# Kernel optimization log

Measured on AMD Instinct MI355X. Metric: run time of the kernel, lower is better.

## Reference

```python
import math
import jax, jax.numpy as jnp
import numpy as np

EMB = 1024
HEADS = 16
HEAD_DIM = EMB // HEADS


def setup_inputs() -> dict:
    key = jax.random.key(0)
    ks = jax.random.split(key, 6)
    b, l = 4, 4096
    x = jax.random.normal(ks[0], (b, l, EMB), dtype=jnp.float32)
    # torch Linear weight shape (out, in); xavier_normal std = sqrt(2/(in+out))
    std = math.sqrt(2.0 / (EMB + EMB))
    Wq = jax.random.normal(ks[1], (EMB, EMB), dtype=jnp.float32) * std
    Wk = jax.random.normal(ks[2], (EMB, EMB), dtype=jnp.float32) * std
    Wv = jax.random.normal(ks[3], (EMB, EMB), dtype=jnp.float32) * std
    Wu = jax.random.normal(ks[4], (EMB, EMB), dtype=jnp.float32) * std
    Wo = jax.random.normal(ks[5], (EMB, EMB), dtype=jnp.float32) * std
    return {"x": x, "Wq": Wq, "Wk": Wk, "Wv": Wv, "Wu": Wu, "Wo": Wo}


def _srms_norm(x, eps=1e-12):
    # SRMSNorm over last dim with scale 1/sqrt(head_dims), computed in fp32
    dtype = x.dtype
    xf = x.astype(jnp.float32)
    scale = 1.0 / math.sqrt(x.shape[-1])
    n = jnp.linalg.norm(xf * scale, axis=-1, keepdims=True)
    return (xf / jnp.maximum(n, eps)).astype(dtype)


def reference(x, Wq, Wk, Wv, Wu, Wo):
    b, l, d = x.shape
    h, hd = HEADS, HEAD_DIM
    scale = math.sqrt(hd)

    def proj(W):
        return jnp.einsum('bld,ed->ble', x, W).reshape(b, l, h, hd).transpose(0, 2, 1, 3)

    q = jax.nn.relu(proj(Wq)) / scale        # (b,h,l,hd)
    k = jax.nn.relu(proj(Wk)) / scale
    v = proj(Wv)
    u = jax.nn.silu(proj(Wu))

    kv = jnp.einsum('bhlk,bhlv->bhkv', k, v)  # (b,h,hd,hd) state
    out = jnp.einsum('bhlk,bhkv->bhlv', q, kv)
    out = _srms_norm(out) * u
    out = out.transpose(0, 2, 1, 3).reshape(b, l, d)
    return jnp.einsum('bld,ed->ble', out, Wo)
```

## Files before the change

kernel.cpp:

```cpp
#include <hip/hip_runtime.h>

typedef _Float16 f16;
typedef _Float16 f16x4 __attribute__((ext_vector_type(4)));
typedef _Float16 f16x8 __attribute__((ext_vector_type(8)));
typedef float f32x4 __attribute__((ext_vector_type(4)));

#define EMB 1024
#define SEQL 4096
#define BATCH 4
#define NH 16
#define HD 64
#define BH 64
#define MROWS 16384
#define KVSPLIT 4

#define GLOAD_LDS(gp, lp) \
    __builtin_amdgcn_global_load_lds((const __attribute__((address_space(1))) void*)(gp), \
                                     (__attribute__((address_space(3))) void*)(lp), 16, 0, 0)

struct WPtrs { const float* p[5]; };

#define NXB (MROWS * EMB / 4 / 256)
#define NWB (5 * EMB * EMB / 4 / 256)
#define NZB (BH * HD * HD / 4 / 256)
__global__ void prep_kernel(const float* __restrict__ x, WPtrs wp,
                            f16* __restrict__ x16, f16* __restrict__ w16,
                            float4* __restrict__ kvz)
{
    int gid = blockIdx.x;
    int t = threadIdx.x;
    if (gid < NXB) {
        int i = gid * 256 + t;
        float4 v = ((const float4*)x)[i];
        f16x4 o = { (f16)v.x, (f16)v.y, (f16)v.z, (f16)v.w };
        ((f16x4*)x16)[i] = o;
    } else if (gid < NXB + NWB) {
        int i = (gid - NXB) * 256 + t;
        int wsel = i >> 18;
        int j = i & 262143;
        float4 v = ((const float4*)wp.p[wsel])[j];
        f16x4 o = { (f16)v.x, (f16)v.y, (f16)v.z, (f16)v.w };
        ((f16x4*)(w16 + (size_t)wsel * EMB * EMB))[j] = o;
    } else {
        int i = (gid - NXB - NWB) * 256 + t;
        kvz[i] = float4{0.f, 0.f, 0.f, 0.f};
    }
}


#define FENCE asm volatile("" ::: "memory")
#define WAITV(N) asm volatile("s_waitcnt vmcnt(" #N ")" ::: "memory")
#define BAR do { FENCE; __builtin_amdgcn_s_barrier(); FENCE; } while (0)

template<int MODE>
__global__ __launch_bounds__(512, 2) void gemm_kernel(
    const f16* __restrict__ A, const f16* __restrict__ Bt,
    void* __restrict__ Cv, int M, int N, int K)
{
    __shared__ f16 As[2][256 * 64];
    __shared__ f16 Bs[2][256 * 64];

    const int tid  = threadIdx.x;
    const int lane = tid & 63;
    const int w    = tid >> 6;
    const int rw   = lane & 15;
    const int quad = lane >> 4;
    const int wm   = w >> 2;
    const int wn   = w & 3;

    const f16* Ap = A;
    const f16* Bp = Bt;
    char* Cp = (char*)Cv;
    bool sel_qu = true;
    int m0, n0;
    if (MODE == 34) {
        int bid = blockIdx.x;
        if (bid < 512) {
            m0 = (bid >> 3) * 256; n0 = (bid & 7) * 256;
        } else {
            bid -= 512;
            m0 = (bid >> 6) * 256; n0 = (bid & 63) * 256;
            Ap = Bt + (size_t)2 * EMB * EMB;
            Bp = A;
            Cp = (char*)Cv + (size_t)2 * MROWS * EMB * 2;
            sel_qu = false;
        }
    } else {
        m0 = blockIdx.y * 256; n0 = blockIdx.x * 256;
    }
    const size_t Ks = (size_t)K;
    const int NT = K >> 6;

    const int srow8 = lane >> 3;
    const int slog  = (lane & 7) ^ srow8;
    const f16* gA = Ap + (size_t)(m0 + w * 8 + srow8) * Ks + slog * 8;
    const f16* gB = Bp + (size_t)(n0 + w * 8 + srow8) * Ks + slog * 8;
    const int lst = w * 512;

#define STAGE_A(H, T, BUF) do { \
    GLOAD_LDS(gA + (size_t)((H) * 128 +  0) * Ks + (T) * 64, &As[BUF][(H) * 8192 + lst]); \
    GLOAD_LDS(gA + (size_t)((H) * 128 + 64) * Ks + (T) * 64, &As[BUF][(H) * 8192 + 4096 + lst]); \
} while (0)
#define STAGE_B(H, T, BUF) do { \
    GLOAD_LDS(gB + (size_t)((H) * 128 +  0) * Ks + (T) * 64, &Bs[BUF][(H) * 8192 + lst]); \
    GLOAD_LDS(gB + (size_t)((H) * 128 + 64) * Ks + (T) * 64, &Bs[BUF][(H) * 8192 + 4096 + lst]); \
} while (0)

    const int rw7   = rw & 7;
    const int s0o   = ( quad      ^ rw7) * 8;
    const int s1o   = ((quad + 4) ^ rw7) * 8;
    const int abase = (wm * 64 + rw) * 64;
    const int bbase = (wn * 32 + rw) * 64;

    f32x4 acc[2][2][4][2] = {};
    f16x8 af[4][2], bf[2][2];

#define READ_A(QM, BUF) do { \
    _Pragma("unroll") \
    for (int mi = 0; mi < 4; ++mi) { \
        af[mi][0] = *(const f16x8*)&As[BUF][(QM) * 8192 + abase + mi * 1024 + s0o]; \
        af[mi][1] = *(const f16x8*)&As[BUF][(QM) * 8192 + abase + mi * 1024 + s1o]; \
    } \
} while (0)
#define READ_B(QN, BUF) do { \
    _Pragma("unroll") \
    for (int nj = 0; nj < 2; ++nj) { \
        bf[nj][0] = *(const f16x8*)&Bs[BUF][(QN) * 8192 + bbase + nj * 1024 + s0o]; \
        bf[nj][1] = *(const f16x8*)&Bs[BUF][(QN) * 8192 + bbase + nj * 1024 + s1o]; \
    } \
} while (0)
#define MFMA_Q(QM, QN) do { \
    __builtin_amdgcn_s_setprio(1); \
    _Pragma("unroll") \
    for (int mi = 0; mi < 4; ++mi) \
        _Pragma("unroll") \
        for (int nj = 0; nj < 2; ++nj) { \
            acc[QM][QN][mi][nj] = __builtin_amdgcn_mfma_f32_16x16x32_f16(bf[nj][0], af[mi][0], acc[QM][QN][mi][nj], 0, 0, 0); \
            acc[QM][QN][mi][nj] = __builtin_amdgcn_mfma_f32_16x16x32_f16(bf[nj][1], af[mi][1], acc[QM][QN][mi][nj], 0, 0, 0); \
        } \
    __builtin_amdgcn_s_setprio(0); \
} while (0)

    STAGE_A(0, 0, 0);
    STAGE_B(0, 0, 0);
    STAGE_B(1, 0, 0);
    STAGE_A(1, 0, 0);
    if (NT > 1) { STAGE_A(0, 1, 1); WAITV(2); } else { WAITV(0); }
    BAR;

    for (int kt = 0; kt < NT; ++kt) {
        const int cur = kt & 1, nxt = cur ^ 1;
        const bool p1 = (kt + 1 < NT), p2 = (kt + 2 < NT);
        READ_A(0, cur); READ_B(0, cur);
        if (p1) STAGE_B(0, kt + 1, nxt);
        BAR; MFMA_Q(0, 0); BAR;
        READ_B(1, cur);
        if (p1) { STAGE_B(1, kt + 1, nxt); WAITV(6); } else { WAITV(0); }
        BAR; MFMA_Q(0, 1); BAR;
        READ_A(1, cur);
        if (p1) STAGE_A(1, kt + 1, nxt);
        BAR; MFMA_Q(1, 1); BAR;
        READ_B(0, cur);
        if (p2) { STAGE_A(0, kt + 2, cur); WAITV(4); }
        else if (p1) { WAITV(2); }
        BAR; MFMA_Q(1, 0); BAR;
    }

    #pragma unroll
    for (int qm = 0; qm < 2; ++qm)
    #pragma unroll
    for (int qn = 0; qn < 2; ++qn)
    #pragma unroll
    for (int mi = 0; mi < 4; ++mi)
    #pragma unroll
    for (int nj = 0; nj < 2; ++nj) {
        const int m_idx = m0 + qm * 128 + wm * 64 + mi * 16 + rw;
        const int n_idx = n0 + qn * 128 + wn * 32 + nj * 16 + quad * 4;
        f32x4 a = acc[qm][qn][mi][nj];
        if (MODE == 0) {
            float4 vv = { a[0], a[1], a[2], a[3] };
            *(float4*)&((float*)Cv)[(size_t)m_idx * N + n_idx] = vv;
        } else if (sel_qu) {
            int sel = n_idx >> 10, e = n_idx & 1023;
            int b = m_idx >> 12, l = m_idx & 4095, h = e >> 6, hdi = e & 63;
            f16x4 o;
            #pragma unroll
            for (int r = 0; r < 4; r++) {
                float v = a[r];
                o[r] = (f16)(sel ? (v / (1.0f + __expf(-v))) : (fmaxf(v, 0.0f) * 0.125f));
            }
            *(f16x4*)&((f16*)Cp)[(size_t)sel * MROWS * EMB +
                                 (((size_t)(b * 16 + h) * 4096 + l) << 6) + hdi] = o;
        } else {
            int sel = m_idx >> 10, e = m_idx & 1023;
            int b = n_idx >> 12, l = n_idx & 4095;
            f16x4 o;
            #pragma unroll
            for (int r = 0; r < 4; r++) {
                float v = a[r];
                o[r] = (f16)(sel ? v : (fmaxf(v, 0.0f) * 0.125f));
            }
            *(f16x4*)&((f16*)Cp)[(size_t)sel * MROWS * EMB +
                                 (((size_t)b * 1024 + e) << 12) + l] = o;
        }
    }
#undef STAGE_A
#undef STAGE_B
#undef READ_A
#undef READ_B
#undef MFMA_Q
}

__global__ __launch_bounds__(256) void kv_split_kernel(
    const f16* __restrict__ kT, const f16* __restrict__ vT, float* __restrict__ kv32)
{
    const int bh    = blockIdx.x;
    const int chunk = blockIdx.y;
    const int lane  = threadIdx.x & 63;
    const int w     = threadIdx.x >> 6;
    const int rw    = lane & 15;
    const int quad  = lane >> 4;
    const int lbase = chunk * (SEQL / KVSPLIT);

    const f16* kp = kT + (size_t)bh * HD * SEQL + (size_t)(w * 16 + rw) * SEQL + lbase + quad * 8;
    const f16* vp = vT + (size_t)bh * HD * SEQL + (size_t)rw * SEQL + lbase + quad * 8;

    f32x4 acc[4] = {};
    for (int k0 = 0; k0 < SEQL / KVSPLIT; k0 += 32) {
        f16x8 a = *(const f16x8*)(kp + k0);
        #pragma unroll
        for (int t = 0; t < 4; t++) {
            f16x8 b = *(const f16x8*)(vp + (size_t)16 * t * SEQL + k0);
            acc[t] = __builtin_amdgcn_mfma_f32_16x16x32_f16(a, b, acc[t], 0, 0, 0);
        }
    }
    float* out = kv32 + (size_t)bh * HD * HD;
    #pragma unroll
    for (int t = 0; t < 4; t++)
        #pragma unroll
        for (int r = 0; r < 4; r++)
            atomicAdd(&out[(w * 16 + quad * 4 + r) * 64 + t * 16 + rw], acc[t][r]);
}

__global__ __launch_bounds__(256) void ret_out_kernel(
    const f16* __restrict__ q, const f16* __restrict__ u,
    const float* __restrict__ kv32, f16* __restrict__ o)
{
    const int bh    = blockIdx.x;
    const int chunk = blockIdx.y;
    const int lane  = threadIdx.x & 63;
    const int w     = threadIdx.x >> 6;
    const int rw    = lane & 15;
    const int quad  = lane >> 4;

    const float* kvp = kv32 + (size_t)bh * 4096;
    f16x8 bf[2][4];
    #pragma unroll
    for (int s = 0; s < 2; s++)
        #pragma unroll
        for (int t = 0; t < 4; t++)
            #pragma unroll
            for (int j = 0; j < 8; j++)
                bf[s][t][j] = (f16)kvp[(s * 32 + quad * 8 + j) * 64 + t * 16 + rw];

    const f16* qp = q + (size_t)bh * SEQL * HD;
    const f16* up = u + (size_t)bh * SEQL * HD;
    const int b = bh >> 4, h = bh & 15;
    f16* op = o + (size_t)b * SEQL * EMB + h * 64;

    const int l_wave = chunk * 512 + w * 128;
    for (int s = 0; s < 8; s++) {
        const int l0 = l_wave + s * 16;
        f16x8 a0 = *(const f16x8*)(qp + (size_t)(l0 + rw) * 64 + quad * 8);
        f16x8 a1 = *(const f16x8*)(qp + (size_t)(l0 + rw) * 64 + 32 + quad * 8);
        f32x4 acc[4] = {};
        #pragma unroll
        for (int t = 0; t < 4; t++) {
            acc[t] = __builtin_amdgcn_mfma_f32_16x16x32_f16(bf[0][t], a0, acc[t], 0, 0, 0);
            acc[t] = __builtin_amdgcn_mfma_f32_16x16x32_f16(bf[1][t], a1, acc[t], 0, 0, 0);
        }
        float ss = 0.f;
        #pragma unroll
        for (int t = 0; t < 4; t++)
            #pragma unroll
            for (int r = 0; r < 4; r++)
                ss += acc[t][r] * acc[t][r];
        ss += __shfl_xor(ss, 16);
        ss += __shfl_xor(ss, 32);
        const float inv = 8.0f / fmaxf(sqrtf(ss), 8e-12f);
        #pragma unroll
        for (int t = 0; t < 4; t++) {
            const int col = t * 16 + quad * 4;
            f16x4 uv = *(const f16x4*)(up + (size_t)(l0 + rw) * 64 + col);
            f16x4 o4;
            #pragma unroll
            for (int r = 0; r < 4; r++)
                o4[r] = (f16)(acc[t][r] * inv * (float)uv[r]);
            *(f16x4*)&op[(size_t)(l0 + rw) * EMB + col] = o4;
        }
    }
}

extern "C" void kernel_launch(void* const* d_in, const int* in_sizes, int n_in,
                              void* d_out, int out_size, void* d_ws, size_t ws_size,
                              hipStream_t stream)
{
    const float* x = (const float*)d_in[0];
    WPtrs wp;
    wp.p[0] = (const float*)d_in[1];
    wp.p[1] = (const float*)d_in[4];
    wp.p[2] = (const float*)d_in[2];
    wp.p[3] = (const float*)d_in[3];
    wp.p[4] = (const float*)d_in[5];

    char* ws = (char*)d_ws;
    size_t off = 0;
    f16* x16 = (f16*)(ws + off); off += (size_t)MROWS * EMB * 2;
    f16* w16 = (f16*)(ws + off); off += (size_t)5 * EMB * EMB * 2;
    f16* qb  = (f16*)(ws + off); off += (size_t)MROWS * EMB * 2;
    f16* ub  = (f16*)(ws + off); off += (size_t)MROWS * EMB * 2;
    f16* kTb = (f16*)(ws + off); off += (size_t)MROWS * EMB * 2;
    f16* vTb = (f16*)(ws + off); off += (size_t)MROWS * EMB * 2;
    float* kv32 = (float*)(ws + off); off += (size_t)BH * HD * HD * 4;
    f16* ob  = x16;
    (void)ub; (void)vTb;

    prep_kernel<<<NXB + NWB + NZB, 256, 0, stream>>>(x, wp, x16, w16, (float4*)kv32);

    f16* Wo = w16 + (size_t)4 * EMB * EMB;

    gemm_kernel<34><<<1024, 512, 0, stream>>>(x16, w16, qb, MROWS, 2 * EMB, EMB);

    kv_split_kernel<<<dim3(BH, KVSPLIT), dim3(256), 0, stream>>>(kTb, vTb, kv32);
    ret_out_kernel<<<dim3(BH, 8), dim3(256), 0, stream>>>(qb, ub, kv32, ob);

    gemm_kernel<0><<<dim3(4, 64), dim3(512), 0, stream>>>(ob, Wo, d_out, MROWS, EMB, EMB);
}
```

Before: 374.3 us.

## Fuse KV reduction, retention output and Wo GEMM into one cooperative kernel

Replaces the kv_split, ret_out and final output GEMM launches with a single cooperative tail kernel of 256 blocks x 512 threads. Grid-wide syncs separate the three phases: atomic KV-state accumulation, the normalized q·kv times u product, and the Wo projection with an LDS double-buffered MFMA loop. This is meant to remove inter-kernel launch gaps and tail effects. In exchange it adds two grid barriers, and it relies on every block being co-resident, given 128KB of static LDS per block.

```diff
diff --git a/kernel.cpp b/kernel.cpp
--- a/kernel.cpp
+++ b/kernel.cpp
@@ -1,4 +1,7 @@
 #include <hip/hip_runtime.h>
+#include <hip/hip_cooperative_groups.h>
+
+namespace cg = cooperative_groups;
 
 typedef _Float16 f16;
 typedef _Float16 f16x4 __attribute__((ext_vector_type(4)));
@@ -12,7 +15,6 @@
 #define HD 64
 #define BH 64
 #define MROWS 16384
-#define KVSPLIT 4
 
 #define GLOAD_LDS(gp, lp) \
     __builtin_amdgcn_global_load_lds((const __attribute__((address_space(1))) void*)(gp), \
@@ -211,93 +213,199 @@
 #undef MFMA_Q
 }
 
-__global__ __launch_bounds__(256) void kv_split_kernel(
-    const f16* __restrict__ kT, const f16* __restrict__ vT, float* __restrict__ kv32)
+__global__ __launch_bounds__(512, 2) void tail_kernel(
+    const f16* __restrict__ kT, const f16* __restrict__ vT, float* __restrict__ kv32,
+    const f16* __restrict__ q, const f16* __restrict__ u, f16* __restrict__ ob,
+    const f16* __restrict__ Wo, float* __restrict__ outp)
 {
-    const int bh    = blockIdx.x;
-    const int chunk = blockIdx.y;
-    const int lane  = threadIdx.x & 63;
-    const int w     = threadIdx.x >> 6;
-    const int rw    = lane & 15;
-    const int quad  = lane >> 4;
-    const int lbase = chunk * (SEQL / KVSPLIT);
-
-    const f16* kp = kT + (size_t)bh * HD * SEQL + (size_t)(w * 16 + rw) * SEQL + lbase + quad * 8;
-    const f16* vp = vT + (size_t)bh * HD * SEQL + (size_t)rw * SEQL + lbase + quad * 8;
-
-    f32x4 acc[4] = {};
-    for (int k0 = 0; k0 < SEQL / KVSPLIT; k0 += 32) {
-        f16x8 a = *(const f16x8*)(kp + k0);
-        #pragma unroll
-        for (int t = 0; t < 4; t++) {
-            f16x8 b = *(const f16x8*)(vp + (size_t)16 * t * SEQL + k0);
-            acc[t] = __builtin_amdgcn_mfma_f32_16x16x32_f16(a, b, acc[t], 0, 0, 0);
-        }
-    }
-    float* out = kv32 + (size_t)bh * HD * HD;
-    #pragma unroll
-    for (int t = 0; t < 4; t++)
-        #pragma unroll
-        for (int r = 0; r < 4; r++)
-            atomicAdd(&out[(w * 16 + quad * 4 + r) * 64 + t * 16 + rw], acc[t][r]);
-}
-
-__global__ __launch_bounds__(256) void ret_out_kernel(
-    const f16* __restrict__ q, const f16* __restrict__ u,
-    const float* __restrict__ kv32, f16* __restrict__ o)
-{
-    const int bh    = blockIdx.x;
-    const int chunk = blockIdx.y;
-    const int lane  = threadIdx.x & 63;
-    const int w     = threadIdx.x >> 6;
-    const int rw    = lane & 15;
-    const int quad  = lane >> 4;
-
-    const float* kvp = kv32 + (size_t)bh * 4096;
-    f16x8 bf[2][4];
-    #pragma unroll
-    for (int s = 0; s < 2; s++)
-        #pragma unroll
-        for (int t = 0; t < 4; t++)
-            #pragma unroll
-            for (int j = 0; j < 8; j++)
-                bf[s][t][j] = (f16)kvp[(s * 32 + quad * 8 + j) * 64 + t * 16 + rw];
-
-    const f16* qp = q + (size_t)bh * SEQL * HD;
-    const f16* up = u + (size_t)bh * SEQL * HD;
-    const int b = bh >> 4, h = bh & 15;
-    f16* op = o + (size_t)b * SEQL * EMB + h * 64;
-
-    const int l_wave = chunk * 512 + w * 128;
-    for (int s = 0; s < 8; s++) {
-        const int l0 = l_wave + s * 16;
-        f16x8 a0 = *(const f16x8*)(qp + (size_t)(l0 + rw) * 64 + quad * 8);
-        f16x8 a1 = *(const f16x8*)(qp + (size_t)(l0 + rw) * 64 + 32 + quad * 8);
-        f32x4 acc[4] = {};
-        #pragma unroll
-        for (int t = 0; t < 4; t++) {
-            acc[t] = __builtin_amdgcn_mfma_f32_16x16x32_f16(bf[0][t], a0, acc[t], 0, 0, 0);
-            acc[t] = __builtin_amdgcn_mfma_f32_16x16x32_f16(bf[1][t], a1, acc[t], 0, 0, 0);
-        }
-        float ss = 0.f;
-        #pragma unroll
-        for (int t = 0; t < 4; t++)
+    __shared__ f16 As[2][256 * 64];
+    __shared__ f16 Bs[2][256 * 64];
+
+    const int tid  = threadIdx.x;
+    const int lane = tid & 63;
+    const int w    = tid >> 6;
+    const int rw   = lane & 15;
+    const int quad = lane >> 4;
+    const int bid  = blockIdx.x;
+    const int bh   = bid >> 2;
+    const int c    = bid & 3;
+
+    {
+        const int mg = w >> 1, nh = w & 1;
+        const int lbase = c * 1024;
+        const f16* kp = kT + (size_t)bh * HD * SEQL + (size_t)(mg * 16 + rw) * SEQL + lbase + quad * 8;
+        const f16* vp = vT + (size_t)bh * HD * SEQL + (size_t)rw * SEQL + lbase + quad * 8;
+        f32x4 acc[2] = {};
+        for (int k0 = 0; k0 < 1024; k0 += 32) {
+            f16x8 a = *(const f16x8*)(kp + k0);
+            #pragma unroll
+            for (int t = 0; t < 2; t++) {
+                f16x8 b = *(const f16x8*)(vp + (size_t)16 * (nh * 2 + t) * SEQL + k0);
+                acc[t] = __builtin_amdgcn_mfma_f32_16x16x32_f16(a, b, acc[t], 0, 0, 0);
+            }
+        }
+        float* o = kv32 + (size_t)bh * HD * HD;
+        #pragma unroll
+        for (int t = 0; t < 2; t++)
             #pragma unroll
             for (int r = 0; r < 4; r++)
-                ss += acc[t][r] * acc[t][r];
-        ss += __shfl_xor(ss, 16);
-        ss += __shfl_xor(ss, 32);
-        const float inv = 8.0f / fmaxf(sqrtf(ss), 8e-12f);
-        #pragma unroll
-        for (int t = 0; t < 4; t++) {
-            const int col = t * 16 + quad * 4;
-            f16x4 uv = *(const f16x4*)(up + (size_t)(l0 + rw) * 64 + col);
-            f16x4 o4;
-            #pragma unroll
-            for (int r = 0; r < 4; r++)
-                o4[r] = (f16)(acc[t][r] * inv * (float)uv[r]);
-            *(f16x4*)&op[(size_t)(l0 + rw) * EMB + col] = o4;
-        }
+                atomicAdd(&o[(mg * 16 + quad * 4 + r) * 64 + (nh * 2 + t) * 16 + rw], acc[t][r]);
+    }
+
+    cg::this_grid().sync();
+
+    {
+        const float* kvp = kv32 + (size_t)bh * 4096;
+        f16x8 bf[2][4];
+        #pragma unroll
+        for (int s = 0; s < 2; s++)
+            #pragma unroll
+            for (int t = 0; t < 4; t++)
+                #pragma unroll
+                for (int j = 0; j < 8; j++)
+                    bf[s][t][j] = (f16)kvp[(s * 32 + quad * 8 + j) * 64 + t * 16 + rw];
+
+        const f16* qp = q + (size_t)bh * SEQL * HD;
+        const f16* up = u + (size_t)bh * SEQL * HD;
+        const int b = bh >> 4, h = bh & 15;
+        f16* op = ob + (size_t)b * SEQL * EMB + h * 64;
+
+        const int l_wave = c * 1024 + w * 128;
+        for (int s = 0; s < 8; s++) {
+            const int l0 = l_wave + s * 16;
+            f16x8 a0 = *(const f16x8*)(qp + (size_t)(l0 + rw) * 64 + quad * 8);
+            f16x8 a1 = *(const f16x8*)(qp + (size_t)(l0 + rw) * 64 + 32 + quad * 8);
+            f32x4 acc[4] = {};
+            #pragma unroll
+            for (int t = 0; t < 4; t++) {
+                acc[t] = __builtin_amdgcn_mfma_f32_16x16x32_f16(bf[0][t], a0, acc[t], 0, 0, 0);
+                acc[t] = __builtin_amdgcn_mfma_f32_16x16x32_f16(bf[1][t], a1, acc[t], 0, 0, 0);
+            }
+            float ss = 0.f;
+            #pragma unroll
+            for (int t = 0; t < 4; t++)
+                #pragma unroll
+                for (int r = 0; r < 4; r++)
+                    ss += acc[t][r] * acc[t][r];
+            ss += __shfl_xor(ss, 16);
+            ss += __shfl_xor(ss, 32);
+            const float inv = 8.0f / fmaxf(sqrtf(ss), 8e-12f);
+            #pragma unroll
+            for (int t = 0; t < 4; t++) {
+                const int col = t * 16 + quad * 4;
+                f16x4 uv = *(const f16x4*)(up + (size_t)(l0 + rw) * 64 + col);
+                f16x4 o4;
+                #pragma unroll
+                for (int r = 0; r < 4; r++)
+                    o4[r] = (f16)(acc[t][r] * inv * (float)uv[r]);
+                *(f16x4*)&op[(size_t)(l0 + rw) * EMB + col] = o4;
+            }
+        }
+    }
+
+    cg::this_grid().sync();
+
+    {
+        const int wm = w >> 2, wn = w & 3;
+        const int m0 = (bid >> 2) * 256;
+        const int n0 = (bid & 3) * 256;
+        const size_t Ks = EMB;
+        const int NT = EMB >> 6;
+
+        const int srow8 = lane >> 3;
+        const int slog  = (lane & 7) ^ srow8;
+        const f16* gA = ob + (size_t)(m0 + w * 8 + srow8) * Ks + slog * 8;
+        const f16* gB = Wo + (size_t)(n0 + w * 8 + srow8) * Ks + slog * 8;
+        const int lst = w * 512;
+
+#define T_STAGE_A(H, T, BUF) do { \
+    GLOAD_LDS(gA + (size_t)((H) * 128 +  0) * Ks + (T) * 64, &As[BUF][(H) * 8192 + lst]); \
+    GLOAD_LDS(gA + (size_t)((H) * 128 + 64) * Ks + (T) * 64, &As[BUF][(H) * 8192 + 4096 + lst]); \
+} while (0)
+#define T_STAGE_B(H, T, BUF) do { \
+    GLOAD_LDS(gB + (size_t)((H) * 128 +  0) * Ks + (T) * 64, &Bs[BUF][(H) * 8192 + lst]); \
+    GLOAD_LDS(gB + (size_t)((H) * 128 + 64) * Ks + (T) * 64, &Bs[BUF][(H) * 8192 + 4096 + lst]); \
+} while (0)
+
+        const int rw7   = rw & 7;
+        const int s0o   = ( quad      ^ rw7) * 8;
+        const int s1o   = ((quad + 4) ^ rw7) * 8;
+        const int abase = (wm * 64 + rw) * 64;
+        const int bbase = (wn * 32 + rw) * 64;
+
+        f32x4 acc[2][2][4][2] = {};
+        f16x8 af[4][2], bf[2][2];
+
+#define T_READ_A(QM, BUF) do { \
+    _Pragma("unroll") \
+    for (int mi = 0; mi < 4; ++mi) { \
+        af[mi][0] = *(const f16x8*)&As[BUF][(QM) * 8192 + abase + mi * 1024 + s0o]; \
+        af[mi][1] = *(const f16x8*)&As[BUF][(QM) * 8192 + abase + mi * 1024 + s1o]; \
+    } \
+} while (0)
+#define T_READ_B(QN, BUF) do { \
+    _Pragma("unroll") \
+    for (int nj = 0; nj < 2; ++nj) { \
+        bf[nj][0] = *(const f16x8*)&Bs[BUF][(QN) * 8192 + bbase + nj * 1024 + s0o]; \
+        bf[nj][1] = *(const f16x8*)&Bs[BUF][(QN) * 8192 + bbase + nj * 1024 + s1o]; \
+    } \
+} while (0)
+#define T_MFMA_Q(QM, QN) do { \
+    __builtin_amdgcn_s_setprio(1); \
+    _Pragma("unroll") \
+    for (int mi = 0; mi < 4; ++mi) \
+        _Pragma("unroll") \
+        for (int nj = 0; nj < 2; ++nj) { \
+            acc[QM][QN][mi][nj] = __builtin_amdgcn_mfma_f32_16x16x32_f16(bf[nj][0], af[mi][0], acc[QM][QN][mi][nj], 0, 0, 0); \
+            acc[QM][QN][mi][nj] = __builtin_amdgcn_mfma_f32_16x16x32_f16(bf[nj][1], af[mi][1], acc[QM][QN][mi][nj], 0, 0, 0); \
+        } \
+    __builtin_amdgcn_s_setprio(0); \
+} while (0)
+
+        T_STAGE_A(0, 0, 0);
+        T_STAGE_B(0, 0, 0);
+        T_STAGE_B(1, 0, 0);
+        T_STAGE_A(1, 0, 0);
+        T_STAGE_A(0, 1, 1); WAITV(2);
+        BAR;
+
+        for (int kt = 0; kt < NT; ++kt) {
+            const int cur = kt & 1, nxt = cur ^ 1;
+            const bool p1 = (kt + 1 < NT), p2 = (kt + 2 < NT);
+            T_READ_A(0, cur); T_READ_B(0, cur);
+            if (p1) T_STAGE_B(0, kt + 1, nxt);
+            BAR; T_MFMA_Q(0, 0); BAR;
+            T_READ_B(1, cur);
+            if (p1) { T_STAGE_B(1, kt + 1, nxt); WAITV(6); } else { WAITV(0); }
+            BAR; T_MFMA_Q(0, 1); BAR;
+            T_READ_A(1, cur);
+            if (p1) T_STAGE_A(1, kt + 1, nxt);
+            BAR; T_MFMA_Q(1, 1); BAR;
+            T_READ_B(0, cur);
+            if (p2) { T_STAGE_A(0, kt + 2, cur); WAITV(4); }
+            else if (p1) { WAITV(2); }
+            BAR; T_MFMA_Q(1, 0); BAR;
+        }
+
+        #pragma unroll
+        for (int qm = 0; qm < 2; ++qm)
+        #pragma unroll
+        for (int qn = 0; qn < 2; ++qn)
+        #pragma unroll
+        for (int mi = 0; mi < 4; ++mi)
+        #pragma unroll
+        for (int nj = 0; nj < 2; ++nj) {
+            const int m_idx = m0 + qm * 128 + wm * 64 + mi * 16 + rw;
+            const int n_idx = n0 + qn * 128 + wn * 32 + nj * 16 + quad * 4;
+            f32x4 a = acc[qm][qn][mi][nj];
+            float4 vv = { a[0], a[1], a[2], a[3] };
+            *(float4*)&outp[(size_t)m_idx * EMB + n_idx] = vv;
+        }
+#undef T_STAGE_A
+#undef T_STAGE_B
+#undef T_READ_A
+#undef T_READ_B
+#undef T_MFMA_Q
     }
 }
 
@@ -323,7 +431,7 @@
     f16* vTb = (f16*)(ws + off); off += (size_t)MROWS * EMB * 2;
     float* kv32 = (float*)(ws + off); off += (size_t)BH * HD * HD * 4;
     f16* ob  = x16;
-    (void)ub; (void)vTb;
+    (void)vTb;
 
     prep_kernel<<<NXB + NWB + NZB, 256, 0, stream>>>(x, wp, x16, w16, (float4*)kv32);
 
@@ -331,8 +439,7 @@
 
     gemm_kernel<34><<<1024, 512, 0, stream>>>(x16, w16, qb, MROWS, 2 * EMB, EMB);
 
-    kv_split_kernel<<<dim3(BH, KVSPLIT), dim3(256), 0, stream>>>(kTb, vTb, kv32);
-    ret_out_kernel<<<dim3(BH, 8), dim3(256), 0, stream>>>(qb, ub, kv32, ob);
-
-    gemm_kernel<0><<<dim3(4, 64), dim3(512), 0, stream>>>(ob, Wo, d_out, MROWS, EMB, EMB);
+    float* outp = (float*)d_out;
+    void* args[] = { &kTb, &vTb, &kv32, &qb, &ub, &ob, &Wo, &outp };
+    hipLaunchCooperativeKernel((void*)tail_kernel, dim3(256), dim3(512), args, 0, stream);
 }
```

Result: slower. 453.6 us (+21.2%).
